# Kernel tuning notes

Measured on AMD Instinct MI355X. Metric: run time of the kernel, lower is better.

Reference implementation:

```python
import jax, jax.numpy as jnp
import numpy as np

N_NODES = 100000
N_EDGES = 1600000
D_IN = 64
D_OUT = 64
BN_EPS = 1e-5


def setup_inputs() -> dict:
    key = jax.random.key(0)
    k_x, k_src, k_dst, k_ew, k_w = jax.random.split(key, 5)
    x = jax.random.normal(k_x, (N_NODES, D_IN), dtype=jnp.float32)
    edge_src = jax.random.randint(k_src, (N_EDGES,), 0, N_NODES, dtype=jnp.int32)
    edge_dst = jax.random.randint(k_dst, (N_EDGES,), 0, N_NODES, dtype=jnp.int32)
    edge_weight = jax.random.uniform(k_ew, (N_EDGES,), dtype=jnp.float32)
    # Xavier-uniform weight, zero bias (reset_parameters)
    limit = float(np.sqrt(6.0 / (D_IN + D_OUT)))
    W = jax.random.uniform(k_w, (D_IN, D_OUT), dtype=jnp.float32, minval=-limit, maxval=limit)
    bias = jnp.zeros((D_OUT,), dtype=jnp.float32)
    gamma = jnp.ones((D_OUT,), dtype=jnp.float32)
    beta = jnp.zeros((D_OUT,), dtype=jnp.float32)
    return {"x": x, "edge_src": edge_src, "edge_dst": edge_dst,
            "edge_weight": edge_weight, "W": W, "bias": bias,
            "gamma": gamma, "beta": beta}


def reference(x, edge_src, edge_dst, edge_weight, W, bias, gamma, beta):
    # GraphConvolution: support = x @ W  -> [N, D_OUT]
    support = jnp.matmul(x, W)
    # spmm(adj, support) with adj in COO form: out[d] += w_e * support[s]
    msgs = edge_weight[:, None] * support[edge_src]        # [E, D_OUT]
    agg = jax.ops.segment_sum(msgs, edge_dst, num_segments=N_NODES)
    out = agg + bias
    # BatchNorm1d (training mode: batch statistics over node dim)
    mean = jnp.mean(out, axis=0)
    var = jnp.var(out, axis=0)
    out = (out - mean) * jax.lax.rsqrt(var + BN_EPS) * gamma + beta
    # ReLU activation; dropout is identity in deterministic/inference mode
    return jax.nn.relu(out)
```

## Files before the change

kernel.cpp:

```cpp
#include <hip/hip_runtime.h>
#include <hip/hip_bf16.h>

#define NN 100000
#define NE 1600000
#define DD 64
#define NCOARSE 196
#define GEMM_TILES 1563
#define PLACE_EPB 2048
#define PLACE_BLOCKS 782
#define LCNT_STRIDE 800
#define STAT_BLOCKS 256

__device__ inline unsigned short f2bf(float f) {
    __hip_bfloat16 h = __float2bfloat16(f);
    unsigned short s; __builtin_memcpy(&s, &h, 2); return s;
}
__device__ inline float pw(unsigned p) { return __uint_as_float((p & 0xFFFE0000u) >> 1); }

__global__ __launch_bounds__(256) void k_hist(const int* __restrict__ edst,
                                              int* __restrict__ lcntT) {
    __shared__ int h[NCOARSE];
    for (int i = threadIdx.x; i < NCOARSE; i += 256) h[i] = 0;
    __syncthreads();
    const int e0 = blockIdx.x * PLACE_EPB;
#pragma unroll
    for (int k = 0; k < 8; ++k) {
        int e = e0 + k * 256 + threadIdx.x;
        if (e < NE) atomicAdd(&h[edst[e] >> 9], 1);
    }
    __syncthreads();
    for (int i = threadIdx.x; i < NCOARSE; i += 256)
        lcntT[i * LCNT_STRIDE + blockIdx.x] = h[i];
}

__global__ __launch_bounds__(256) void k_colscan(int* __restrict__ lcntT,
                                                 int* __restrict__ cnt) {
    int* col = lcntT + blockIdx.x * LCNT_STRIDE;
    const int t = threadIdx.x, base = t * 4;
    int v[4], s = 0;
#pragma unroll
    for (int j = 0; j < 4; ++j) {
        v[j] = (base + j < PLACE_BLOCKS) ? col[base + j] : 0;
        s += v[j];
    }
    __shared__ int sc[256];
    sc[t] = s; __syncthreads();
    for (int o = 1; o < 256; o <<= 1) {
        int u = (t >= o) ? sc[t - o] : 0;
        __syncthreads();
        sc[t] += u;
        __syncthreads();
    }
    int run = sc[t] - s;
#pragma unroll
    for (int j = 0; j < 4; ++j) {
        if (base + j < PLACE_BLOCKS) col[base + j] = run;
        run += v[j];
    }
    if (t == 255) cnt[blockIdx.x] = sc[255];
}

__global__ __launch_bounds__(256) void k_scan196(const int* __restrict__ cnt,
                                                 int* __restrict__ cstart,
                                                 int* __restrict__ bstart) {
    __shared__ int sc[256];
    const int t = threadIdx.x;
    const int v = (t < NCOARSE) ? cnt[t] : 0;
    sc[t] = v; __syncthreads();
    for (int o = 1; o < 256; o <<= 1) {
        int u = (t >= o) ? sc[t - o] : 0;
        __syncthreads();
        sc[t] += u;
        __syncthreads();
    }
    if (t < NCOARSE) cstart[t] = sc[t] - v;
    if (t == 0) { cstart[NCOARSE] = NE; bstart[NN] = NE; }
}

__global__ __launch_bounds__(256) void k_gemm_scatter(const float* __restrict__ x,
                                                      const float* __restrict__ Wg,
                                                      unsigned* __restrict__ support2,
                                                      const int* __restrict__ esrc,
                                                      const int* __restrict__ edst,
                                                      const float* __restrict__ ew,
                                                      const int* __restrict__ cstart,
                                                      const int* __restrict__ lcntT,
                                                      int2* __restrict__ permA) {
    if (blockIdx.x >= GEMM_TILES) {
        const int blk = blockIdx.x - GEMM_TILES;
        __shared__ int loff[NCOARSE];
        for (int i = threadIdx.x; i < NCOARSE; i += 256)
            loff[i] = cstart[i] + lcntT[i * LCNT_STRIDE + blk];
        __syncthreads();
        const int e0 = blk * PLACE_EPB;
#pragma unroll
        for (int k = 0; k < 8; ++k) {
            int e = e0 + k * 256 + threadIdx.x;
            if (e < NE) {
                int d = edst[e];
                int p = atomicAdd(&loff[d >> 9], 1);
                permA[p] = make_int2(esrc[e] | ((d & 511) << 17), __float_as_int(ew[e]));
            }
        }
        return;
    }

    __shared__ float Ws[DD * DD];
    __shared__ float Xs[64 * DD];
    const int r0 = blockIdx.x * 64;
    const int nrows = (r0 + 64 <= NN) ? 64 : (NN - r0);

    for (int i = threadIdx.x; i < DD * DD / 4; i += 256)
        ((float4*)Ws)[i] = ((const float4*)Wg)[i];
    const float4* xg = (const float4*)(x + (size_t)r0 * DD);
    for (int i = threadIdx.x; i < nrows * 16; i += 256)
        ((float4*)Xs)[i] = xg[i];
    __syncthreads();

    const int wave = threadIdx.x >> 6, lane = threadIdx.x & 63;
    const int half = lane >> 5, hl = lane & 31;
    const int rbase = wave * 16 + half * 8;

    float acc0[8] = {0.f, 0.f, 0.f, 0.f, 0.f, 0.f, 0.f, 0.f};
    float acc1[8] = {0.f, 0.f, 0.f, 0.f, 0.f, 0.f, 0.f, 0.f};
#pragma unroll 4
    for (int k = 0; k < DD; k += 4) {
        float2 w0 = *(const float2*)&Ws[(k + 0) * DD + 2 * hl];
        float2 w1 = *(const float2*)&Ws[(k + 1) * DD + 2 * hl];
        float2 w2 = *(const float2*)&Ws[(k + 2) * DD + 2 * hl];
        float2 w3 = *(const float2*)&Ws[(k + 3) * DD + 2 * hl];
#pragma unroll
        for (int r = 0; r < 8; ++r) {
            float4 xv = *(const float4*)&Xs[(rbase + r) * DD + k];
            acc0[r] = fmaf(xv.x, w0.x, acc0[r]); acc1[r] = fmaf(xv.x, w0.y, acc1[r]);
            acc0[r] = fmaf(xv.y, w1.x, acc0[r]); acc1[r] = fmaf(xv.y, w1.y, acc1[r]);
            acc0[r] = fmaf(xv.z, w2.x, acc0[r]); acc1[r] = fmaf(xv.z, w2.y, acc1[r]);
            acc0[r] = fmaf(xv.w, w3.x, acc0[r]); acc1[r] = fmaf(xv.w, w3.y, acc1[r]);
        }
    }
#pragma unroll
    for (int r = 0; r < 8; ++r) {
        const int row = rbase + r;
        if (row < nrows) {
            unsigned p = (unsigned)f2bf(acc0[r]) | ((unsigned)f2bf(acc1[r]) << 16);
            support2[(size_t)(r0 + row) * 32 + hl] = p;
        }
    }
}

__global__ __launch_bounds__(1024) void k_placeB(const int* __restrict__ cstart,
                                                 const int2* __restrict__ permA,
                                                 unsigned* __restrict__ perm,
                                                 int* __restrict__ bstart) {
    __shared__ int sc[512], loff[512], wtot[8];
    const int c = blockIdx.x, t = threadIdx.x;
    const int wave = t >> 6, lane = t & 63;
    const int cs = cstart[c], ce = cstart[c + 1];
    if (t < 512) sc[t] = 0;
    __syncthreads();
    for (int j = cs + t; j < ce; j += 1024)
        atomicAdd(&sc[(permA[j].x >> 17) & 511], 1);
    __syncthreads();
    int v = 0, xv = 0;
    if (wave < 8) {
        v = sc[t];
        xv = v;
#pragma unroll
        for (int o = 1; o < 64; o <<= 1) {
            int u = __shfl_up(xv, o, 64);
            if (lane >= o) xv += u;
        }
        if (lane == 63) wtot[wave] = xv;
    }
    __syncthreads();
    if (t < 8) {
        int w = wtot[t], xw = w;
#pragma unroll
        for (int o = 1; o < 8; o <<= 1) {
            int u = __shfl_up(xw, o, 64);
            if (t >= o) xw += u;
        }
        wtot[t] = xw - w;
    }
    __syncthreads();
    if (wave < 8) {
        const int base = cs + wtot[wave] + xv - v;
        loff[t] = base;
        const int node = c * 512 + t;
        if (node < NN) bstart[node] = base;
    }
    __syncthreads();
    for (int j = cs + t; j < ce; j += 1024) {
        int2 m = permA[j];
        int p = atomicAdd(&loff[(m.x >> 17) & 511], 1);
        unsigned wb = (unsigned)(f2bf(__int_as_float(m.y)) & 0x7FFF);
        perm[p] = (unsigned)(m.x & 0x1FFFF) | (wb << 17);
    }
}

__global__ __launch_bounds__(512) void k_gather(const int* __restrict__ bstart,
                                                const unsigned* __restrict__ perm,
                                                const uint4* __restrict__ support4,
                                                float* __restrict__ out) {
    const int wave = threadIdx.x >> 6, lane = threadIdx.x & 63;
    const int sub = lane >> 3, q = lane & 7;
    const int d = blockIdx.x * 8 + wave;
    const int bs = bstart[d], be = bstart[d + 1];
    float acc[8] = {0.f, 0.f, 0.f, 0.f, 0.f, 0.f, 0.f, 0.f};
    int j0 = bs;
    for (; j0 + 15 < be; j0 += 16) {
        unsigned mA = perm[j0 + sub];
        unsigned mB = perm[j0 + 8 + sub];
        uint4 pA = support4[(size_t)(mA & 0x1FFFF) * 8 + q];
        uint4 pB = support4[(size_t)(mB & 0x1FFFF) * 8 + q];
        float wA = pw(mA), wB = pw(mB);
        acc[0] = fmaf(wA, __uint_as_float(pA.x << 16), acc[0]);
        acc[1] = fmaf(wA, __uint_as_float(pA.x & 0xffff0000u), acc[1]);
        acc[2] = fmaf(wA, __uint_as_float(pA.y << 16), acc[2]);
        acc[3] = fmaf(wA, __uint_as_float(pA.y & 0xffff0000u), acc[3]);
        acc[4] = fmaf(wA, __uint_as_float(pA.z << 16), acc[4]);
        acc[5] = fmaf(wA, __uint_as_float(pA.z & 0xffff0000u), acc[5]);
        acc[6] = fmaf(wA, __uint_as_float(pA.w << 16), acc[6]);
        acc[7] = fmaf(wA, __uint_as_float(pA.w & 0xffff0000u), acc[7]);
        acc[0] = fmaf(wB, __uint_as_float(pB.x << 16), acc[0]);
        acc[1] = fmaf(wB, __uint_as_float(pB.x & 0xffff0000u), acc[1]);
        acc[2] = fmaf(wB, __uint_as_float(pB.y << 16), acc[2]);
        acc[3] = fmaf(wB, __uint_as_float(pB.y & 0xffff0000u), acc[3]);
        acc[4] = fmaf(wB, __uint_as_float(pB.z << 16), acc[4]);
        acc[5] = fmaf(wB, __uint_as_float(pB.z & 0xffff0000u), acc[5]);
        acc[6] = fmaf(wB, __uint_as_float(pB.w << 16), acc[6]);
        acc[7] = fmaf(wB, __uint_as_float(pB.w & 0xffff0000u), acc[7]);
    }
    for (; j0 < be; j0 += 8) {
        if (j0 + sub < be) {
            unsigned m = perm[j0 + sub];
            uint4 p = support4[(size_t)(m & 0x1FFFF) * 8 + q];
            float w = pw(m);
            acc[0] = fmaf(w, __uint_as_float(p.x << 16), acc[0]);
            acc[1] = fmaf(w, __uint_as_float(p.x & 0xffff0000u), acc[1]);
            acc[2] = fmaf(w, __uint_as_float(p.y << 16), acc[2]);
            acc[3] = fmaf(w, __uint_as_float(p.y & 0xffff0000u), acc[3]);
            acc[4] = fmaf(w, __uint_as_float(p.z << 16), acc[4]);
            acc[5] = fmaf(w, __uint_as_float(p.z & 0xffff0000u), acc[5]);
            acc[6] = fmaf(w, __uint_as_float(p.w << 16), acc[6]);
            acc[7] = fmaf(w, __uint_as_float(p.w & 0xffff0000u), acc[7]);
        }
    }
#pragma unroll
    for (int i = 0; i < 8; ++i) {
        acc[i] += __shfl_xor(acc[i], 8, 64);
        acc[i] += __shfl_xor(acc[i], 16, 64);
        acc[i] += __shfl_xor(acc[i], 32, 64);
    }
    if (sub == 0) {
        float* op = out + (size_t)d * DD + q * 8;
        *(float4*)op = make_float4(acc[0], acc[1], acc[2], acc[3]);
        *(float4*)(op + 4) = make_float4(acc[4], acc[5], acc[6], acc[7]);
    }
}

__device__ inline float4 shfl_down4(float4 v, int dd) {
    v.x = __shfl_down(v.x, dd, 64); v.y = __shfl_down(v.y, dd, 64);
    v.z = __shfl_down(v.z, dd, 64); v.w = __shfl_down(v.w, dd, 64);
    return v;
}
__device__ inline float4 add4(float4 a, float4 b) {
    a.x += b.x; a.y += b.y; a.z += b.z; a.w += b.w; return a;
}

__global__ __launch_bounds__(256) void k_stats(const float* __restrict__ agg,
                                               float* __restrict__ pstat) {
    const int lane = threadIdx.x & 63, wave = threadIdx.x >> 6;
    const int q = lane & 15, sub = lane >> 4;
    float4 s = {0, 0, 0, 0}, sq = {0, 0, 0, 0};
    const int stride = gridDim.x * 16;
    for (int row = (blockIdx.x * 4 + wave) * 4 + sub; row < NN; row += stride) {
        float4 v = *(const float4*)(agg + (size_t)row * DD + q * 4);
        s.x += v.x; s.y += v.y; s.z += v.z; s.w += v.w;
        sq.x = fmaf(v.x, v.x, sq.x); sq.y = fmaf(v.y, v.y, sq.y);
        sq.z = fmaf(v.z, v.z, sq.z); sq.w = fmaf(v.w, v.w, sq.w);
    }
    s = add4(s, shfl_down4(s, 32));  s = add4(s, shfl_down4(s, 16));
    sq = add4(sq, shfl_down4(sq, 32)); sq = add4(sq, shfl_down4(sq, 16));

    __shared__ float red[2][4][DD];
    if (lane < 16) {
        red[0][wave][q * 4 + 0] = s.x;  red[0][wave][q * 4 + 1] = s.y;
        red[0][wave][q * 4 + 2] = s.z;  red[0][wave][q * 4 + 3] = s.w;
        red[1][wave][q * 4 + 0] = sq.x; red[1][wave][q * 4 + 1] = sq.y;
        red[1][wave][q * 4 + 2] = sq.z; red[1][wave][q * 4 + 3] = sq.w;
    }
    __syncthreads();
    if (threadIdx.x < 2 * DD) {
        const int t = threadIdx.x;
        const int part = t >> 6, c = t & 63;
        pstat[blockIdx.x * 2 * DD + t] =
            red[part][0][c] + red[part][1][c] + red[part][2][c] + red[part][3][c];
    }
}

__global__ __launch_bounds__(128) void k_finstats(const float* __restrict__ pstat,
                                                  float* __restrict__ ss,
                                                  const float* __restrict__ gamma,
                                                  const float* __restrict__ beta) {
    const int t = threadIdx.x;
    float acc = 0.f;
    for (int b = 0; b < STAT_BLOCKS; ++b)
        acc += pstat[b * 2 * DD + t];
    __shared__ float red[2 * DD];
    red[t] = acc;
    __syncthreads();
    if (t < DD) {
        const float invn = 1.0f / NN;
        float mean = red[t] * invn;
        float var = fmaxf(red[DD + t] * invn - mean * mean, 0.f);
        float sc = rsqrtf(var + 1e-5f) * gamma[t];
        ss[t] = sc;
        ss[DD + t] = beta[t] - mean * sc;
    }
}

__global__ __launch_bounds__(256) void k_final(float* __restrict__ out,
                                               const float* __restrict__ ss) {
    const size_t idx = ((size_t)blockIdx.x * 256 + threadIdx.x) * 4;
    const int c = (int)(idx & 63);
    float4 v = *(const float4*)(out + idx);
    float4 o;
    o.x = fmaxf(fmaf(v.x, ss[c + 0], ss[DD + c + 0]), 0.f);
    o.y = fmaxf(fmaf(v.y, ss[c + 1], ss[DD + c + 1]), 0.f);
    o.z = fmaxf(fmaf(v.z, ss[c + 2], ss[DD + c + 2]), 0.f);
    o.w = fmaxf(fmaf(v.w, ss[c + 3], ss[DD + c + 3]), 0.f);
    *(float4*)(out + idx) = o;
}

extern "C" void kernel_launch(void* const* d_in, const int* in_sizes, int n_in,
                              void* d_out, int out_size, void* d_ws, size_t ws_size,
                              hipStream_t stream) {
    const float* x     = (const float*)d_in[0];
    const int*   esrc  = (const int*)d_in[1];
    const int*   edst  = (const int*)d_in[2];
    const float* ew    = (const float*)d_in[3];
    const float* W     = (const float*)d_in[4];
    const float* gamma = (const float*)d_in[6];
    const float* beta  = (const float*)d_in[7];
    float*       out   = (float*)d_out;

    char* ws = (char*)d_ws;
    unsigned* support2 = (unsigned*)ws;  ws += (size_t)NN * DD * 2;
    int2*     permA  = (int2*)ws;     ws += (size_t)NE * 8;
    unsigned* perm   = (unsigned*)ws; ws += (size_t)NE * 4;
    int*   lcntT  = (int*)ws;    ws += NCOARSE * LCNT_STRIDE * 4;
    int*   cnt    = (int*)ws;    ws += NCOARSE * 4;
    float* ss     = (float*)ws;  ws += 128 * 4;
    int*   cstart = (int*)ws;    ws += (NCOARSE + 1) * 4;
    int*   bstart = (int*)ws;    ws += (NN + 4) * 4;
    float* pstat  = (float*)ws;  ws += STAT_BLOCKS * 2 * DD * 4;

    k_hist        <<<PLACE_BLOCKS, 256, 0, stream>>>(edst, lcntT);
    k_colscan     <<<NCOARSE, 256, 0, stream>>>(lcntT, cnt);
    k_scan196     <<<1, 256, 0, stream>>>(cnt, cstart, bstart);
    k_gemm_scatter<<<GEMM_TILES + PLACE_BLOCKS, 256, 0, stream>>>(
                      x, W, support2, esrc, edst, ew, cstart, lcntT, permA);
    k_placeB      <<<NCOARSE, 1024, 0, stream>>>(cstart, permA, perm, bstart);
    k_gather      <<<NN / 8, 512, 0, stream>>>(bstart, perm, (const uint4*)support2, out);
    k_stats       <<<STAT_BLOCKS, 256, 0, stream>>>(out, pstat);
    k_finstats    <<<1, 128, 0, stream>>>(pstat, ss, gamma, beta);
    k_final       <<<NN * DD / 4 / 256, 256, 0, stream>>>(out, ss);
}
```

Measured before the change: 212.9 us.

## Fuse BatchNorm statistics into gather kernel and shrink GEMM tiles

The gather kernel now computes per-block column sums and sums of squares from its register accumulators and writes per-block partials. This removes the separate stats kernel that re-read the whole aggregated output. A new two-level reduction (k_pred, then k_finstats) folds the 12500 partials. The GEMM tile also shrinks from 64 to 32 rows per block, giving more blocks and dropping the tail bounds check since 32 divides the node count. This adds an extra kernel launch and more partial traffic.

```diff
diff --git a/kernel.cpp b/kernel.cpp
--- a/kernel.cpp
+++ b/kernel.cpp
@@ -5,11 +5,12 @@
 #define NE 1600000
 #define DD 64
 #define NCOARSE 196
-#define GEMM_TILES 1563
+#define GEMM_TILES 3125
 #define PLACE_EPB 2048
 #define PLACE_BLOCKS 782
 #define LCNT_STRIDE 800
-#define STAT_BLOCKS 256
+#define GATHER_BLOCKS 12500
+#define PRED_BLOCKS 125
 
 __device__ inline unsigned short f2bf(float f) {
     __hip_bfloat16 h = __float2bfloat16(f);
@@ -106,23 +107,22 @@
     }
 
     __shared__ float Ws[DD * DD];
-    __shared__ float Xs[64 * DD];
-    const int r0 = blockIdx.x * 64;
-    const int nrows = (r0 + 64 <= NN) ? 64 : (NN - r0);
+    __shared__ float Xs[32 * DD];
+    const int r0 = blockIdx.x * 32;
 
     for (int i = threadIdx.x; i < DD * DD / 4; i += 256)
         ((float4*)Ws)[i] = ((const float4*)Wg)[i];
     const float4* xg = (const float4*)(x + (size_t)r0 * DD);
-    for (int i = threadIdx.x; i < nrows * 16; i += 256)
+    for (int i = threadIdx.x; i < 32 * 16; i += 256)
         ((float4*)Xs)[i] = xg[i];
     __syncthreads();
 
     const int wave = threadIdx.x >> 6, lane = threadIdx.x & 63;
     const int half = lane >> 5, hl = lane & 31;
-    const int rbase = wave * 16 + half * 8;
-
-    float acc0[8] = {0.f, 0.f, 0.f, 0.f, 0.f, 0.f, 0.f, 0.f};
-    float acc1[8] = {0.f, 0.f, 0.f, 0.f, 0.f, 0.f, 0.f, 0.f};
+    const int rbase = wave * 8 + half * 4;
+
+    float acc0[4] = {0.f, 0.f, 0.f, 0.f};
+    float acc1[4] = {0.f, 0.f, 0.f, 0.f};
 #pragma unroll 4
     for (int k = 0; k < DD; k += 4) {
         float2 w0 = *(const float2*)&Ws[(k + 0) * DD + 2 * hl];
@@ -130,7 +130,7 @@
         float2 w2 = *(const float2*)&Ws[(k + 2) * DD + 2 * hl];
         float2 w3 = *(const float2*)&Ws[(k + 3) * DD + 2 * hl];
 #pragma unroll
-        for (int r = 0; r < 8; ++r) {
+        for (int r = 0; r < 4; ++r) {
             float4 xv = *(const float4*)&Xs[(rbase + r) * DD + k];
             acc0[r] = fmaf(xv.x, w0.x, acc0[r]); acc1[r] = fmaf(xv.x, w0.y, acc1[r]);
             acc0[r] = fmaf(xv.y, w1.x, acc0[r]); acc1[r] = fmaf(xv.y, w1.y, acc1[r]);
@@ -139,12 +139,9 @@
         }
     }
 #pragma unroll
-    for (int r = 0; r < 8; ++r) {
-        const int row = rbase + r;
-        if (row < nrows) {
-            unsigned p = (unsigned)f2bf(acc0[r]) | ((unsigned)f2bf(acc1[r]) << 16);
-            support2[(size_t)(r0 + row) * 32 + hl] = p;
-        }
+    for (int r = 0; r < 4; ++r) {
+        unsigned p = (unsigned)f2bf(acc0[r]) | ((unsigned)f2bf(acc1[r]) << 16);
+        support2[(size_t)(r0 + rbase + r) * 32 + hl] = p;
     }
 }
 
@@ -201,7 +198,8 @@
 __global__ __launch_bounds__(512) void k_gather(const int* __restrict__ bstart,
                                                 const unsigned* __restrict__ perm,
                                                 const uint4* __restrict__ support4,
-                                                float* __restrict__ out) {
+                                                float* __restrict__ out,
+                                                float* __restrict__ pstat) {
     const int wave = threadIdx.x >> 6, lane = threadIdx.x & 63;
     const int sub = lane >> 3, q = lane & 7;
     const int d = blockIdx.x * 8 + wave;
@@ -252,61 +250,50 @@
         acc[i] += __shfl_xor(acc[i], 16, 64);
         acc[i] += __shfl_xor(acc[i], 32, 64);
     }
+
+    __shared__ float red[2][8][DD];
     if (sub == 0) {
         float* op = out + (size_t)d * DD + q * 8;
         *(float4*)op = make_float4(acc[0], acc[1], acc[2], acc[3]);
         *(float4*)(op + 4) = make_float4(acc[4], acc[5], acc[6], acc[7]);
-    }
-}
-
-__device__ inline float4 shfl_down4(float4 v, int dd) {
-    v.x = __shfl_down(v.x, dd, 64); v.y = __shfl_down(v.y, dd, 64);
-    v.z = __shfl_down(v.z, dd, 64); v.w = __shfl_down(v.w, dd, 64);
-    return v;
-}
-__device__ inline float4 add4(float4 a, float4 b) {
-    a.x += b.x; a.y += b.y; a.z += b.z; a.w += b.w; return a;
-}
-
-__global__ __launch_bounds__(256) void k_stats(const float* __restrict__ agg,
-                                               float* __restrict__ pstat) {
-    const int lane = threadIdx.x & 63, wave = threadIdx.x >> 6;
-    const int q = lane & 15, sub = lane >> 4;
-    float4 s = {0, 0, 0, 0}, sq = {0, 0, 0, 0};
-    const int stride = gridDim.x * 16;
-    for (int row = (blockIdx.x * 4 + wave) * 4 + sub; row < NN; row += stride) {
-        float4 v = *(const float4*)(agg + (size_t)row * DD + q * 4);
-        s.x += v.x; s.y += v.y; s.z += v.z; s.w += v.w;
-        sq.x = fmaf(v.x, v.x, sq.x); sq.y = fmaf(v.y, v.y, sq.y);
-        sq.z = fmaf(v.z, v.z, sq.z); sq.w = fmaf(v.w, v.w, sq.w);
-    }
-    s = add4(s, shfl_down4(s, 32));  s = add4(s, shfl_down4(s, 16));
-    sq = add4(sq, shfl_down4(sq, 32)); sq = add4(sq, shfl_down4(sq, 16));
-
-    __shared__ float red[2][4][DD];
-    if (lane < 16) {
-        red[0][wave][q * 4 + 0] = s.x;  red[0][wave][q * 4 + 1] = s.y;
-        red[0][wave][q * 4 + 2] = s.z;  red[0][wave][q * 4 + 3] = s.w;
-        red[1][wave][q * 4 + 0] = sq.x; red[1][wave][q * 4 + 1] = sq.y;
-        red[1][wave][q * 4 + 2] = sq.z; red[1][wave][q * 4 + 3] = sq.w;
+#pragma unroll
+        for (int i = 0; i < 8; ++i) {
+            red[0][wave][q * 8 + i] = acc[i];
+            red[1][wave][q * 8 + i] = acc[i] * acc[i];
+        }
     }
     __syncthreads();
     if (threadIdx.x < 2 * DD) {
-        const int t = threadIdx.x;
-        const int part = t >> 6, c = t & 63;
-        pstat[blockIdx.x * 2 * DD + t] =
-            red[part][0][c] + red[part][1][c] + red[part][2][c] + red[part][3][c];
-    }
-}
-
-__global__ __launch_bounds__(128) void k_finstats(const float* __restrict__ pstat,
+        const int t = threadIdx.x, part = t >> 6, c = t & 63;
+        float v = 0.f;
+#pragma unroll
+        for (int w = 0; w < 8; ++w) v += red[part][w][c];
+        pstat[(size_t)blockIdx.x * 2 * DD + t] = v;
+    }
+}
+
+__global__ __launch_bounds__(128) void k_pred(const float* __restrict__ pstat,
+                                              float* __restrict__ pstat2) {
+    const int t = threadIdx.x;
+    const float* p = pstat + (size_t)blockIdx.x * 100 * 2 * DD;
+    float a0 = 0.f, a1 = 0.f, a2 = 0.f, a3 = 0.f;
+    for (int r = 0; r < 100; r += 4) {
+        a0 += p[(r + 0) * 2 * DD + t];
+        a1 += p[(r + 1) * 2 * DD + t];
+        a2 += p[(r + 2) * 2 * DD + t];
+        a3 += p[(r + 3) * 2 * DD + t];
+    }
+    pstat2[blockIdx.x * 2 * DD + t] = (a0 + a1) + (a2 + a3);
+}
+
+__global__ __launch_bounds__(128) void k_finstats(const float* __restrict__ pstat2,
                                                   float* __restrict__ ss,
                                                   const float* __restrict__ gamma,
                                                   const float* __restrict__ beta) {
     const int t = threadIdx.x;
     float acc = 0.f;
-    for (int b = 0; b < STAT_BLOCKS; ++b)
-        acc += pstat[b * 2 * DD + t];
+    for (int b = 0; b < PRED_BLOCKS; ++b)
+        acc += pstat2[b * 2 * DD + t];
     __shared__ float red[2 * DD];
     red[t] = acc;
     __syncthreads();
@@ -354,7 +341,8 @@
     float* ss     = (float*)ws;  ws += 128 * 4;
     int*   cstart = (int*)ws;    ws += (NCOARSE + 1) * 4;
     int*   bstart = (int*)ws;    ws += (NN + 4) * 4;
-    float* pstat  = (float*)ws;  ws += STAT_BLOCKS * 2 * DD * 4;
+    float* pstat  = (float*)ws;  ws += (size_t)GATHER_BLOCKS * 2 * DD * 4;
+    float* pstat2 = (float*)ws;  ws += PRED_BLOCKS * 2 * DD * 4;
 
     k_hist        <<<PLACE_BLOCKS, 256, 0, stream>>>(edst, lcntT);
     k_colscan     <<<NCOARSE, 256, 0, stream>>>(lcntT, cnt);
@@ -362,8 +350,8 @@
     k_gemm_scatter<<<GEMM_TILES + PLACE_BLOCKS, 256, 0, stream>>>(
                       x, W, support2, esrc, edst, ew, cstart, lcntT, permA);
     k_placeB      <<<NCOARSE, 1024, 0, stream>>>(cstart, permA, perm, bstart);
-    k_gather      <<<NN / 8, 512, 0, stream>>>(bstart, perm, (const uint4*)support2, out);
-    k_stats       <<<STAT_BLOCKS, 256, 0, stream>>>(out, pstat);
-    k_finstats    <<<1, 128, 0, stream>>>(pstat, ss, gamma, beta);
+    k_gather      <<<GATHER_BLOCKS, 512, 0, stream>>>(bstart, perm, (const uint4*)support2, out, pstat);
+    k_pred        <<<PRED_BLOCKS, 128, 0, stream>>>(pstat, pstat2);
+    k_finstats    <<<1, 128, 0, stream>>>(pstat2, ss, gamma, beta);
     k_final       <<<NN * DD / 4 / 256, 256, 0, stream>>>(out, ss);
 }
```

New measurement: 217.7 us. +2.3%, slower.
